# Performance work log

Measured on AMD Instinct MI355X. Metric: run time of the kernel, lower is better.

## Reference

```python
import jax, jax.numpy as jnp
import numpy as np

N = 32768   # total nodes
B = 128     # graphs
S = 256     # nodes per graph (equal-size graphs)
E = 524288  # edges
DIN = 128   # in_dim
DH = 256    # hidden_dim
H = 8       # heads
DFF = 1024  # ffn hidden
EPS = 1e-5


def _seg_sum(x, idx, num):
    return jax.ops.segment_sum(x, idx, num_segments=num)


def _bn(x, g, b):
    # BatchNorm1d with batch statistics (training-mode math, deterministic)
    mu = jnp.mean(x, axis=0)
    var = jnp.mean((x - mu) ** 2, axis=0)
    return (x - mu) * jax.lax.rsqrt(var + EPS) * g + b


def _ln(x, g, b):
    mu = jnp.mean(x, axis=-1, keepdims=True)
    var = jnp.mean((x - mu) ** 2, axis=-1, keepdims=True)
    return (x - mu) * jax.lax.rsqrt(var + EPS) * g + b


def _gcn_conv(x, W, bias, edge_index, n):
    # PyG GCNConv: h = x W; add self-loops; norm = d^-1/2[row] * d^-1/2[col]; scatter-add at col
    h = x @ W
    loop = jnp.arange(n)
    row = jnp.concatenate([edge_index[0], loop])
    col = jnp.concatenate([edge_index[1], loop])
    deg = _seg_sum(jnp.ones_like(col, dtype=h.dtype), col, n)  # >=1 due to self-loops
    dis = jax.lax.rsqrt(jnp.maximum(deg, 1.0))
    norm = dis[row] * dis[col]
    out = _seg_sum(h[row] * norm[:, None], col, n)
    return out + bias


def setup_inputs() -> dict:
    key = jax.random.key(0)
    ks = jax.random.split(key, 24)

    def w(i, shape, scale=0.05):
        return jax.random.normal(ks[i], shape, dtype=jnp.float32) * scale

    return {
        "x": jax.random.normal(ks[0], (N, DIN), dtype=jnp.float32),
        "edge_index": jax.random.randint(ks[1], (2, E), 0, N, dtype=jnp.int32),
        "batch": jnp.repeat(jnp.arange(B, dtype=jnp.int32), S),
        "inter_f": jax.random.normal(ks[2], (B, DH), dtype=jnp.float32),
        "bn1_g": jnp.ones((DIN,), jnp.float32), "bn1_b": jnp.zeros((DIN,), jnp.float32),
        "bn2_g": jnp.ones((DH,), jnp.float32), "bn2_b": jnp.zeros((DH,), jnp.float32),
        "w_conv1": w(3, (DIN, DH)), "b_conv1": jnp.zeros((DH,), jnp.float32),
        "w_conv2": w(4, (DH, DH)), "b_conv2": jnp.zeros((DH,), jnp.float32),
        "wq": w(5, (DH, DH)), "bq": jnp.zeros((DH,), jnp.float32),
        "wk": w(6, (DH, DH)), "bk": jnp.zeros((DH,), jnp.float32),
        "wv": w(7, (DH, DH)), "bv": jnp.zeros((DH,), jnp.float32),
        "wo": w(8, (DH, DH)), "bo": jnp.zeros((DH,), jnp.float32),
        "ln1_g": jnp.ones((DH,), jnp.float32), "ln1_b": jnp.zeros((DH,), jnp.float32),
        "ln2_g": jnp.ones((DH,), jnp.float32), "ln2_b": jnp.zeros((DH,), jnp.float32),
        "w_ff1": w(9, (DH, DFF)), "b_ff1": jnp.zeros((DFF,), jnp.float32),
        "w_ff2": w(10, (DFF, DH)), "b_ff2": jnp.zeros((DH,), jnp.float32),
    }


def reference(x, edge_index, batch, inter_f,
              bn1_g, bn1_b, bn2_g, bn2_b,
              w_conv1, b_conv1, w_conv2, b_conv2,
              wq, bq, wk, bk, wv, bv, wo, bo,
              ln1_g, ln1_b, ln2_g, ln2_b,
              w_ff1, b_ff1, w_ff2, b_ff2):
    n = x.shape[0]
    hd = DH // H
    # init_avg_h: scatter-mean of raw x per graph
    cnt = _seg_sum(jnp.ones((n,), x.dtype), batch, B)
    init_avg_h = _seg_sum(x, batch, B) / jnp.maximum(cnt, 1.0)[:, None]
    # layer 1 (dropout = identity in eval)
    h = _bn(x, bn1_g, bn1_b)
    h = jax.nn.relu(_gcn_conv(h, w_conv1, b_conv1, edge_index, n))
    # layer 2 with residual
    pre = h
    h2 = _bn(h, bn2_g, bn2_b)
    h = pre + jax.nn.relu(_gcn_conv(h2, w_conv2, b_conv2, edge_index, n))
    # transformer block: inject per-graph feature, self-attend within each graph
    inter_h = inter_f[batch]
    t = (h + inter_h).reshape(B, S, DH)
    q = (t @ wq + bq).reshape(B, S, H, hd)
    k = (t @ wk + bk).reshape(B, S, H, hd)
    v = (t @ wv + bv).reshape(B, S, H, hd)
    scores = jnp.einsum('bqhd,bkhd->bhqk', q, k) / jnp.sqrt(jnp.float32(hd))
    attn = jax.nn.softmax(scores, axis=-1)
    o = jnp.einsum('bhqk,bkhd->bqhd', attn, v).reshape(B, S, DH) @ wo + bo
    t2 = _ln(t + o, ln1_g, ln1_b)
    ffn = jax.nn.relu(t2 @ w_ff1 + b_ff1) @ w_ff2 + b_ff2
    t3 = _ln(t2 + ffn, ln2_g, ln2_b)
    hg = t3.reshape(n, DH)
    readout = _seg_sum(hg, batch, B)
    return readout, init_avg_h
```

## Files before the change

kernel.cpp:

```cpp
#include <hip/hip_runtime.h>
#include <math.h>

#define NN   32768
#define BG   128
#define SG   256
#define EE   524288
#define DIN_ 128
#define DH_  256
#define NH   8
#define HD_  32
#define DFF_ 1024
#define EPS_ 1e-5f

typedef __attribute__((ext_vector_type(8))) short bf16x8;
typedef __attribute__((ext_vector_type(4))) float f32x4;
typedef __attribute__((ext_vector_type(2))) unsigned int u32x2;
typedef __attribute__((ext_vector_type(4))) unsigned int u32x4;

__device__ __forceinline__ unsigned short f2bf(float f) {
    unsigned int u = __builtin_bit_cast(unsigned int, f);
    unsigned int r = u + 0x7FFFu + ((u >> 16) & 1u);
    return (unsigned short)(r >> 16);
}
__device__ __forceinline__ float bf2f(unsigned short u) {
    return __builtin_bit_cast(float, (unsigned int)u << 16);
}
__device__ __forceinline__ unsigned int pack2bf(float a, float b) {
    return (unsigned int)f2bf(a) | ((unsigned int)f2bf(b) << 16);
}
__device__ __forceinline__ void glds16(const unsigned short* g, unsigned short* l) {
    __builtin_amdgcn_global_load_lds(
        (const __attribute__((address_space(1))) void*)g,
        (__attribute__((address_space(3))) void*)l, 16, 0, 0);
}
#define WAIT_VM2() __builtin_amdgcn_s_waitcnt(0x0F72)
#define WAIT_VM1() __builtin_amdgcn_s_waitcnt(0x0F71)
#define WAIT_VM0() __builtin_amdgcn_s_waitcnt(0x0F70)

#define QSCALE (0.17677669529663689f * 1.4426950408889634f)

__global__ __launch_bounds__(128) void initavg_kernel(const float* __restrict__ X,
                                                      float* __restrict__ out2) {
    int b = blockIdx.x, j = threadIdx.x;
    float s = 0.f;
    for (int r = 0; r < SG; ++r) s += X[(size_t)(b * SG + r) * DIN_ + j];
    out2[b * DIN_ + j] = s * (1.f / (float)SG);
}

template <int C>
__global__ __launch_bounds__(C) void colstats_kernel(const float* __restrict__ X,
                                                     float* __restrict__ csum,
                                                     float* __restrict__ csumsq) {
    int j = threadIdx.x;
    size_t r0 = (size_t)blockIdx.x * 256;
    float s = 0.f, sq = 0.f;
    for (int r = 0; r < 256; ++r) {
        float v = X[(r0 + r) * C + j];
        s += v; sq += v * v;
    }
    atomicAdd(&csum[j], s);
    atomicAdd(&csumsq[j], sq);
}

template <int C>
__global__ __launch_bounds__(C) void colstats_b_kernel(const unsigned short* __restrict__ X,
                                                       float* __restrict__ csum,
                                                       float* __restrict__ csumsq) {
    int j = threadIdx.x;
    size_t r0 = (size_t)blockIdx.x * 256;
    float s = 0.f, sq = 0.f;
    for (int r = 0; r < 256; ++r) {
        float v = bf2f(X[(r0 + r) * C + j]);
        s += v; sq += v * v;
    }
    atomicAdd(&csum[j], s);
    atomicAdd(&csumsq[j], sq);
}

template <int C>
__global__ __launch_bounds__(C) void bnfin_kernel(const float* __restrict__ csum,
                                                  const float* __restrict__ csumsq,
                                                  const float* __restrict__ g,
                                                  const float* __restrict__ b,
                                                  float* __restrict__ scale,
                                                  float* __restrict__ shift) {
    int j = threadIdx.x;
    float mu  = csum[j] * (1.f / (float)NN);
    float var = csumsq[j] * (1.f / (float)NN) - mu * mu;
    float s = g[j] * rsqrtf(var + EPS_);
    scale[j] = s;
    shift[j] = b[j] - mu * s;
}

template <int C>
__global__ __launch_bounds__(256) void bnapply_kernel(const float* __restrict__ X,
                                                      const float* __restrict__ sc,
                                                      const float* __restrict__ sh,
                                                      unsigned short* __restrict__ Y) {
    int i = blockIdx.x * 256 + threadIdx.x;
    int j = i & (C - 1);
    Y[i] = f2bf(X[i] * sc[j] + sh[j]);
}

__global__ __launch_bounds__(256) void wtrans_kernel(const float* __restrict__ W,
                                                     unsigned short* __restrict__ Wt,
                                                     int K, int N, float scale) {
    int idx = blockIdx.x * 256 + threadIdx.x;
    if (idx < K * N) {
        int n = idx / K, k = idx - n * K;
        Wt[idx] = f2bf(W[(size_t)k * N + n] * scale);
    }
}

__global__ __launch_bounds__(256) void bcat_kernel(const float* __restrict__ bq,
                                                   const float* __restrict__ bk,
                                                   const float* __restrict__ bv,
                                                   float* __restrict__ o) {
    int j = threadIdx.x;
    if (blockIdx.x == 0) o[j] = bq[j] * QSCALE;
    else if (blockIdx.x == 1) o[DH_ + j] = bk[j];
    else o[2 * DH_ + j] = bv[j];
}

__global__ __launch_bounds__(256) void deg_kernel(const int* __restrict__ col,
                                                  int* __restrict__ deg) {
    int e = blockIdx.x * 256 + threadIdx.x;
    if (e < EE) atomicAdd(&deg[col[e]], 1);
}

__global__ __launch_bounds__(1024) void scan_kernel(const int* __restrict__ deg,
                                                    int* __restrict__ off,
                                                    float* __restrict__ dis) {
    __shared__ int sums[1024];
    int t = threadIdx.x;
    int base = t * 32;
    int loc[32];
    int run = 0;
#pragma unroll
    for (int i = 0; i < 32; ++i) { loc[i] = run; run += deg[base + i]; }
    sums[t] = run;
    __syncthreads();
    for (int d = 1; d < 1024; d <<= 1) {
        int tmp = (t >= d) ? sums[t - d] : 0;
        __syncthreads();
        sums[t] += tmp;
        __syncthreads();
    }
    int excl = sums[t] - run;
#pragma unroll
    for (int i = 0; i < 32; ++i) {
        off[base + i] = excl + loc[i];
        dis[base + i] = rsqrtf((float)(deg[base + i] + 1));
    }
    if (t == 1023) off[NN] = sums[1023];
}

__global__ __launch_bounds__(256) void scatter_kernel(const int* __restrict__ row,
                                                      const int* __restrict__ col,
                                                      const int* __restrict__ off,
                                                      int* __restrict__ cnt,
                                                      int* __restrict__ srow) {
    int e = blockIdx.x * 256 + threadIdx.x;
    if (e < EE) {
        int c = col[e];
        int p = off[c] + atomicAdd(&cnt[c], 1);
        srow[p] = row[e];
    }
}

template <int C, int FUSE_BN>
__global__ __launch_bounds__(256) void aggb_kernel(const unsigned short* __restrict__ X,
                                                   const int* __restrict__ off,
                                                   const int* __restrict__ srow,
                                                   const float* __restrict__ dis,
                                                   const float* __restrict__ scl,
                                                   const float* __restrict__ shf,
                                                   unsigned short* __restrict__ Y) {
    constexpr int EPL = C / 64;
    int lane = threadIdx.x & 63;
    int c = blockIdx.x * 4 + (threadIdx.x >> 6);
    float dc = dis[c];
    float acc[EPL];
    float wsum = dc;
    {
        unsigned short t[EPL];
        const unsigned short* xc = X + (size_t)c * C + lane * EPL;
        if constexpr (EPL == 4) *(uint2*)t = *(const uint2*)xc;
        else *(unsigned int*)t = *(const unsigned int*)xc;
#pragma unroll
        for (int e2 = 0; e2 < EPL; ++e2) acc[e2] = dc * bf2f(t[e2]);
    }
    int s = off[c], en = off[c + 1];
    int i = s;
    for (; i + 4 <= en; i += 4) {
        int r0 = srow[i], r1 = srow[i + 1], r2 = srow[i + 2], r3 = srow[i + 3];
        float d0 = dis[r0], d1 = dis[r1], d2 = dis[r2], d3 = dis[r3];
        unsigned short t0[EPL], t1[EPL], t2[EPL], t3[EPL];
        const unsigned short* p0 = X + (size_t)r0 * C + lane * EPL;
        const unsigned short* p1 = X + (size_t)r1 * C + lane * EPL;
        const unsigned short* p2 = X + (size_t)r2 * C + lane * EPL;
        const unsigned short* p3 = X + (size_t)r3 * C + lane * EPL;
        if constexpr (EPL == 4) {
            *(uint2*)t0 = *(const uint2*)p0;
            *(uint2*)t1 = *(const uint2*)p1;
            *(uint2*)t2 = *(const uint2*)p2;
            *(uint2*)t3 = *(const uint2*)p3;
        } else {
            *(unsigned int*)t0 = *(const unsigned int*)p0;
            *(unsigned int*)t1 = *(const unsigned int*)p1;
            *(unsigned int*)t2 = *(const unsigned int*)p2;
            *(unsigned int*)t3 = *(const unsigned int*)p3;
        }
        wsum += d0 + d1 + d2 + d3;
#pragma unroll
        for (int e2 = 0; e2 < EPL; ++e2) {
            acc[e2] += d0 * bf2f(t0[e2]) + d1 * bf2f(t1[e2]) +
                       d2 * bf2f(t2[e2]) + d3 * bf2f(t3[e2]);
        }
    }
    for (; i < en; ++i) {
        int r = srow[i];
        float dr = dis[r];
        unsigned short t[EPL];
        const unsigned short* xr = X + (size_t)r * C + lane * EPL;
        if constexpr (EPL == 4) *(uint2*)t = *(const uint2*)xr;
        else *(unsigned int*)t = *(const unsigned int*)xr;
        wsum += dr;
#pragma unroll
        for (int e2 = 0; e2 < EPL; ++e2) acc[e2] += dr * bf2f(t[e2]);
    }
    unsigned short t[EPL];
#pragma unroll
    for (int e2 = 0; e2 < EPL; ++e2) {
        float v;
        if constexpr (FUSE_BN) {
            int j = lane * EPL + e2;
            v = dc * (scl[j] * acc[e2] + shf[j] * wsum);
        } else {
            v = dc * acc[e2];
        }
        t[e2] = f2bf(v);
    }
    unsigned short* yc = Y + (size_t)c * C + lane * EPL;
    if constexpr (EPL == 4) *(uint2*)yc = *(const uint2*)t;
    else *(unsigned int*)yc = *(const unsigned int*)t;
}

template <int MT>
__global__ __launch_bounds__(512, 8) void gemm_bf16_kernel(
    const unsigned short* __restrict__ A,
    const unsigned short* __restrict__ Bt,
    unsigned short* __restrict__ Cb,
    int M, int K, int N,
    const float* __restrict__ bias,
    const unsigned short* __restrict__ resb,
    const float* __restrict__ inter,
    int do_relu, int relu_first) {
    constexpr int LDP = 32;
    constexpr int CP = 136;
    constexpr int MI = MT / 64;
    constexpr int ASZ = MT * 32;
    constexpr int SMEMSZ = (MT == 128) ? 128 * CP : 2 * ASZ + 2 * 4096;
    __shared__ unsigned short Smem[SMEMSZ];
    unsigned short* As0 = Smem;
    unsigned short* As1 = Smem + ASZ;
    unsigned short* Bs0 = Smem + 2 * ASZ;
    unsigned short* Bs1 = Smem + 2 * ASZ + 4096;
    unsigned short* Cs  = Smem;
    int gx = gridDim.x, gyP = gridDim.y >> 3;
    int d = blockIdx.y * gx + blockIdx.x;
    int xcd = d & 7, j2 = d >> 3;
    int bm = (xcd * gyP + j2 / gx) * MT;
    int bn = (j2 % gx) * 128;
    int tid = threadIdx.x;
    int wave = tid >> 6, lane = tid & 63;
    int wm = (wave >> 1) * (MT / 4);
    int wn = (wave & 1) * 64;
    int lrc = lane & 15;
    int koct = lane >> 4;
    int rsw = (lrc >> 1) & 3;
    int rofs = (koct ^ rsw) * 8;

    int cg = (lane & 3) ^ ((lane >> 3) & 3);
    int skk = cg * 8;
    const unsigned short* g0 = nullptr;
    unsigned short* l0a = nullptr;
    unsigned short* l0b = nullptr;
    int nloads;
    size_t gstride16;
    if constexpr (MT == 128) {
        int sr = wave * 16 + (lane >> 2);
        g0 = A + (size_t)(bm + sr) * K + skk;
        nloads = 2;
        (void)l0a; (void)l0b; (void)gstride16;
    } else {
        if (wave < 4) {
            int sr = wave * 32 + (lane >> 2);
            g0 = Bt + (size_t)(bn + sr) * K + skk;
            l0a = Bs0 + wave * 1024 + lane * 8;
            l0b = Bs1 + wave * 1024 + lane * 8;
            nloads = 2;
            gstride16 = (size_t)16 * K;
        } else {
            int sr = (wave - 4) * 16 + (lane >> 2);
            g0 = A + (size_t)(bm + sr) * K + skk;
            l0a = As0 + (wave - 4) * 512 + lane * 8;
            l0b = As1 + (wave - 4) * 512 + lane * 8;
            nloads = 1;
            gstride16 = 0;
        }
    }
    const unsigned short* gA0 = nullptr;
    const unsigned short* gB0 = nullptr;
    int lofs = 0;
    if constexpr (MT == 128) {
        int sr = wave * 16 + (lane >> 2);
        gA0 = A + (size_t)(bm + sr) * K + skk;
        gB0 = Bt + (size_t)(bn + sr) * K + skk;
        lofs = wave * 512 + lane * 8;
    }

    f32x4 acc[MI][4];
#pragma unroll
    for (int i = 0; i < MI; ++i)
#pragma unroll
        for (int j = 0; j < 4; ++j) acc[i][j] = (f32x4){0.f, 0.f, 0.f, 0.f};

    if constexpr (MT == 128) {
        glds16(gA0, As0 + lofs);
        glds16(gB0, Bs0 + lofs);
    } else {
        glds16(g0, l0a);
        if (nloads == 2) glds16(g0 + gstride16, l0a + 512);
    }

    int buf = 0;
    for (int k0 = 0; k0 < K; k0 += 32) {
        int nk = k0 + 32;
        if (nk < K) {
            if constexpr (MT == 128) {
                glds16(gA0 + nk, (buf ? As0 : As1) + lofs);
                glds16(gB0 + nk, (buf ? Bs0 : Bs1) + lofs);
                WAIT_VM2();
            } else {
                unsigned short* ln = buf ? l0a : l0b;
                glds16(g0 + nk, ln);
                if (nloads == 2) {
                    glds16(g0 + nk + gstride16, ln + 512);
                    WAIT_VM2();
                } else {
                    WAIT_VM1();
                }
            }
        } else {
            WAIT_VM0();
        }
        __builtin_amdgcn_s_barrier();
        const unsigned short* Ab = buf ? As1 : As0;
        const unsigned short* Bb = buf ? Bs1 : Bs0;
        bf16x8 af[MI], bfr[4];
#pragma unroll
        for (int i = 0; i < MI; ++i)
            af[i] = *(const bf16x8*)(Ab + (wm + i * 16 + lrc) * LDP + rofs);
#pragma unroll
        for (int j = 0; j < 4; ++j)
            bfr[j] = *(const bf16x8*)(Bb + (wn + j * 16 + lrc) * LDP + rofs);
#pragma unroll
        for (int i = 0; i < MI; ++i)
#pragma unroll
            for (int j = 0; j < 4; ++j)
                acc[i][j] = __builtin_amdgcn_mfma_f32_16x16x32_bf16(af[i], bfr[j],
                                                                    acc[i][j], 0, 0, 0);
        __builtin_amdgcn_s_barrier();
        buf ^= 1;
    }
#pragma unroll
    for (int i = 0; i < MI; ++i) {
#pragma unroll
        for (int r = 0; r < 4; ++r) {
            int lrow = wm + i * 16 + koct * 4 + r;
            int grow = bm + lrow;
#pragma unroll
            for (int j = 0; j < 4; ++j) {
                int lcol = wn + j * 16 + lrc;
                int gcol = bn + lcol;
                float v = acc[i][j][r];
                if (bias) v += bias[gcol];
                if (relu_first) v = fmaxf(v, 0.f);
                if (resb) v += bf2f(resb[(size_t)grow * N + gcol]);
                if (inter) v += inter[(grow >> 8) * N + gcol];
                if (do_relu && !relu_first) v = fmaxf(v, 0.f);
                Cs[lrow * CP + lcol] = f2bf(v);
            }
        }
    }
    __syncthreads();
#pragma unroll
    for (int it = 0; it < MT / 32; ++it) {
        int row = it * 32 + (tid >> 4);
        int cc = (tid & 15) * 8;
        *(uint4*)(&Cb[(size_t)(bm + row) * N + bn + cc]) =
            *(const uint4*)(&Cs[row * CP + cc]);
    }
}

__global__ __launch_bounds__(256, 4) void attn_mfma_kernel(
    const unsigned short* __restrict__ QKV,
    unsigned short* __restrict__ Ob) {
    int b = blockIdx.x >> 3, h = blockIdx.x & 7;
    __shared__ unsigned short Ks[256 * 32];
    __shared__ unsigned short Vt[32 * 264];
    __shared__ float Lc[4 * 64];
    const unsigned short* kg = QKV + (size_t)b * 256 * 768 + 256 + h * 32;
    const unsigned short* vg = QKV + (size_t)b * 256 * 768 + 512 + h * 32;
    int tid = threadIdx.x;
#pragma unroll
    for (int it = 0; it < 4; ++it) {
        int c = it * 256 + tid;
        int row = c >> 2, ch = c & 3;
        int slot = ch ^ ((row >> 1) & 3);
        *(uint4*)(Ks + row * 32 + slot * 8) =
            *(const uint4*)(kg + (size_t)row * 768 + ch * 8);
    }
#pragma unroll
    for (int it = 0; it < 4; ++it) {
        int c = it * 256 + tid;
        int key = c >> 2, d0 = (c & 3) * 8;
        unsigned short tmp[8];
        *(uint4*)tmp = *(const uint4*)(vg + (size_t)key * 768 + d0);
#pragma unroll
        for (int j = 0; j < 8; ++j) Vt[(d0 + j) * 264 + key] = tmp[j];
    }
    __syncthreads();

    int wave = tid >> 6, lane = tid & 63;
    int lr = lane & 15, koct = lane >> 4;
    int s4 = (lr >> 1) & 3;
    int qrow0 = b * 256 + wave * 64;
    bf16x8 qf[4];
#pragma unroll
    for (int j = 0; j < 4; ++j)
        qf[j] = *(const bf16x8*)(QKV + (size_t)(qrow0 + j * 16 + lr) * 768 + h * 32 + koct * 8);

    f32x4 Oa[4][2];
    float lp[4];
#pragma unroll
    for (int i = 0; i < 4; ++i) {
        Oa[i][0] = (f32x4){0.f, 0.f, 0.f, 0.f};
        Oa[i][1] = (f32x4){0.f, 0.f, 0.f, 0.f};
        lp[i] = 0.f;
    }
    float* Lw = Lc + wave * 64;

    for (int kc = 0; kc < 256; kc += 32) {
        bf16x8 kf0 = *(const bf16x8*)(Ks + (kc + lr) * 32 + (koct ^ s4) * 8);
        bf16x8 kf1 = *(const bf16x8*)(Ks + (kc + 16 + lr) * 32 + (koct ^ s4) * 8);
        bf16x8 pfr[4];
#pragma unroll
        for (int j = 0; j < 4; ++j) {
            f32x4 St0 = __builtin_amdgcn_mfma_f32_16x16x32_bf16(kf0, qf[j],
                            (f32x4){0.f, 0.f, 0.f, 0.f}, 0, 0, 0);
            f32x4 St1 = __builtin_amdgcn_mfma_f32_16x16x32_bf16(kf1, qf[j],
                            (f32x4){0.f, 0.f, 0.f, 0.f}, 0, 0, 0);
            float p0[4], p1[4], ps = 0.f;
#pragma unroll
            for (int r = 0; r < 4; ++r) {
                p0[r] = exp2f(St0[r]); p1[r] = exp2f(St1[r]);
                ps += p0[r] + p1[r];
            }
            lp[j] += ps;
            unsigned int w0a, w0b, w1a, w1b;
            asm("v_cvt_pk_bf16_f32 %0, %1, %2" : "=v"(w0a) : "v"(p0[0]), "v"(p0[1]));
            asm("v_cvt_pk_bf16_f32 %0, %1, %2" : "=v"(w0b) : "v"(p0[2]), "v"(p0[3]));
            asm("v_cvt_pk_bf16_f32 %0, %1, %2" : "=v"(w1a) : "v"(p1[0]), "v"(p1[1]));
            asm("v_cvt_pk_bf16_f32 %0, %1, %2" : "=v"(w1b) : "v"(p1[2]), "v"(p1[3]));
            u32x2 sa = __builtin_amdgcn_permlane32_swap(w0a, w1a, false, false);
            u32x2 da = __builtin_amdgcn_permlane16_swap(sa[0], sa[1], false, false);
            u32x2 sb = __builtin_amdgcn_permlane32_swap(w0b, w1b, false, false);
            u32x2 db = __builtin_amdgcn_permlane16_swap(sb[0], sb[1], false, false);
            u32x4 pw = {da[0], db[0], da[1], db[1]};
            pfr[j] = __builtin_bit_cast(bf16x8, pw);
        }
        bf16x8 vf0 = *(const bf16x8*)(Vt + lr * 264 + kc + koct * 8);
        bf16x8 vf1 = *(const bf16x8*)(Vt + (16 + lr) * 264 + kc + koct * 8);
#pragma unroll
        for (int i = 0; i < 4; ++i) {
            Oa[i][0] = __builtin_amdgcn_mfma_f32_16x16x32_bf16(pfr[i], vf0, Oa[i][0], 0, 0, 0);
            Oa[i][1] = __builtin_amdgcn_mfma_f32_16x16x32_bf16(pfr[i], vf1, Oa[i][1], 0, 0, 0);
        }
    }
#pragma unroll
    for (int j = 0; j < 4; ++j) {
        lp[j] += __shfl_xor(lp[j], 16);
        lp[j] += __shfl_xor(lp[j], 32);
    }
    if (koct == 0) {
#pragma unroll
        for (int j = 0; j < 4; ++j) Lw[j * 16 + lr] = lp[j];
    }
    __builtin_amdgcn_s_waitcnt(0);
#pragma unroll
    for (int i = 0; i < 4; ++i) {
        f32x4 l4 = *(const f32x4*)(Lw + i * 16 + koct * 4);
#pragma unroll
        for (int r = 0; r < 4; ++r) {
            float inv = 1.f / l4[r];
            int row = qrow0 + i * 16 + koct * 4 + r;
#pragma unroll
            for (int jn = 0; jn < 2; ++jn) {
                int col = h * 32 + jn * 16 + lr;
                Ob[(size_t)row * 256 + col] = f2bf(Oa[i][jn][r] * inv);
            }
        }
    }
}

__global__ __launch_bounds__(256) void lnb_kernel(const unsigned short* __restrict__ Z,
                                                  unsigned short* __restrict__ Out,
                                                  const float* __restrict__ g,
                                                  const float* __restrict__ bt) {
    int row = blockIdx.x * 4 + (threadIdx.x >> 6);
    int lane = threadIdx.x & 63;
    const unsigned short* z = Z + (size_t)row * DH_;
    float v[4];
    float sum = 0.f;
#pragma unroll
    for (int i = 0; i < 4; ++i) { v[i] = bf2f(z[lane + i * 64]); sum += v[i]; }
#pragma unroll
    for (int off = 32; off; off >>= 1) sum += __shfl_xor(sum, off);
    float mu = sum * (1.f / (float)DH_);
    float vs = 0.f;
#pragma unroll
    for (int i = 0; i < 4; ++i) { float d = v[i] - mu; vs += d * d; }
#pragma unroll
    for (int off = 32; off; off >>= 1) vs += __shfl_xor(vs, off);
    float rs = rsqrtf(vs * (1.f / (float)DH_) + EPS_);
#pragma unroll
    for (int i = 0; i < 4; ++i) {
        int col = lane + i * 64;
        Out[(size_t)row * DH_ + col] = f2bf((v[i] - mu) * rs * g[col] + bt[col]);
    }
}

__global__ __launch_bounds__(256) void readout_kernel(const unsigned short* __restrict__ T3,
                                                      float* __restrict__ out) {
    int b = blockIdx.x, j = threadIdx.x;
    float s = 0.f;
    for (int r = 0; r < SG; ++r) s += bf2f(T3[(size_t)(b * SG + r) * DH_ + j]);
    out[b * DH_ + j] = s;
}

extern "C" void kernel_launch(void* const* d_in, const int* in_sizes, int n_in,
                              void* d_out, int out_size, void* d_ws, size_t ws_size,
                              hipStream_t stream) {
    const float* x       = (const float*)d_in[0];
    const int*   ei      = (const int*)d_in[1];
    const float* inter_f = (const float*)d_in[3];
    const float* bn1_g = (const float*)d_in[4],  *bn1_b = (const float*)d_in[5];
    const float* bn2_g = (const float*)d_in[6],  *bn2_b = (const float*)d_in[7];
    const float* w_conv1 = (const float*)d_in[8],  *b_conv1 = (const float*)d_in[9];
    const float* w_conv2 = (const float*)d_in[10], *b_conv2 = (const float*)d_in[11];
    const float* wq = (const float*)d_in[12], *bq = (const float*)d_in[13];
    const float* wk = (const float*)d_in[14], *bk = (const float*)d_in[15];
    const float* wv = (const float*)d_in[16], *bv = (const float*)d_in[17];
    const float* wo = (const float*)d_in[18], *bo = (const float*)d_in[19];
    const float* ln1_g = (const float*)d_in[20], *ln1_b = (const float*)d_in[21];
    const float* ln2_g = (const float*)d_in[22], *ln2_b = (const float*)d_in[23];
    const float* w_ff1 = (const float*)d_in[24], *b_ff1 = (const float*)d_in[25];
    const float* w_ff2 = (const float*)d_in[26], *b_ff2 = (const float*)d_in[27];
    float* out = (float*)d_out;

    char* base = (char*)d_ws;
    size_t o = 0;
    auto alloc = [&](size_t bytes) -> void* {
        void* p = base + o;
        o = (o + bytes + 255) & ~(size_t)255;
        return p;
    };
    int*   deg    = (int*)alloc(NN * 4);
    int*   off    = (int*)alloc((NN + 1) * 4);
    int*   cnt    = (int*)alloc(NN * 4);
    int*   srow   = (int*)alloc(EE * 4);
    float* dis    = (float*)alloc(NN * 4);
    float* csum   = (float*)alloc(256 * 4);
    float* csumsq = (float*)alloc(256 * 4);
    float* scl    = (float*)alloc(256 * 4);
    float* shf    = (float*)alloc(256 * 4);
    float* bqkv   = (float*)alloc(768 * 4);
    const size_t SLOT = (size_t)NN * DH_;
    unsigned short* Arena = (unsigned short*)alloc((size_t)NN * DFF_ * 2);
    unsigned short* TB = (unsigned short*)alloc(SLOT * 2);
    unsigned short* B0 = (unsigned short*)alloc(SLOT * 2);
    unsigned short* wc1t  = (unsigned short*)alloc((size_t)DIN_ * DH_ * 2);
    unsigned short* wc2t  = (unsigned short*)alloc((size_t)DH_ * DH_ * 2);
    unsigned short* wqkvt = (unsigned short*)alloc((size_t)DH_ * DH_ * 3 * 2);
    unsigned short* wot   = (unsigned short*)alloc((size_t)DH_ * DH_ * 2);
    unsigned short* wf1t  = (unsigned short*)alloc((size_t)DH_ * DFF_ * 2);
    unsigned short* wf2t  = (unsigned short*)alloc((size_t)DFF_ * DH_ * 2);
    unsigned short* Xa   = Arena;
    unsigned short* X2a  = Arena + (size_t)NN * DIN_;
    unsigned short* QKVb = Arena;
    unsigned short* zb   = Arena + SLOT * 3;
    unsigned short* Fb   = Arena;
    unsigned short* tb   = TB;
    unsigned short* z2b  = TB;

    hipMemsetAsync(deg, 0, NN * 4, stream);
    hipMemsetAsync(cnt, 0, NN * 4, stream);
    hipMemsetAsync(csum, 0, 2048, stream);

    wtrans_kernel<<<(DIN_ * DH_ + 255) / 256, 256, 0, stream>>>(w_conv1, wc1t, DIN_, DH_, 1.f);
    wtrans_kernel<<<(DH_ * DH_ + 255) / 256, 256, 0, stream>>>(w_conv2, wc2t, DH_, DH_, 1.f);
    wtrans_kernel<<<(DH_ * DH_ + 255) / 256, 256, 0, stream>>>(wq, wqkvt, DH_, DH_, QSCALE);
    wtrans_kernel<<<(DH_ * DH_ + 255) / 256, 256, 0, stream>>>(wk, wqkvt + DH_ * DH_, DH_, DH_, 1.f);
    wtrans_kernel<<<(DH_ * DH_ + 255) / 256, 256, 0, stream>>>(wv, wqkvt + 2 * DH_ * DH_, DH_, DH_, 1.f);
    wtrans_kernel<<<(DH_ * DH_ + 255) / 256, 256, 0, stream>>>(wo, wot, DH_, DH_, 1.f);
    wtrans_kernel<<<(DH_ * DFF_ + 255) / 256, 256, 0, stream>>>(w_ff1, wf1t, DH_, DFF_, 1.f);
    wtrans_kernel<<<(DFF_ * DH_ + 255) / 256, 256, 0, stream>>>(w_ff2, wf2t, DFF_, DH_, 1.f);
    bcat_kernel<<<3, 256, 0, stream>>>(bq, bk, bv, bqkv);

    initavg_kernel<<<BG, 128, 0, stream>>>(x, out + BG * DH_);

    colstats_kernel<DIN_><<<NN / 256, DIN_, 0, stream>>>(x, csum, csumsq);
    bnfin_kernel<DIN_><<<1, DIN_, 0, stream>>>(csum, csumsq, bn1_g, bn1_b, scl, shf);
    bnapply_kernel<DIN_><<<NN * DIN_ / 256, 256, 0, stream>>>(x, scl, shf, B0);

    deg_kernel<<<EE / 256, 256, 0, stream>>>(ei + EE, deg);
    scan_kernel<<<1, 1024, 0, stream>>>(deg, off, dis);
    scatter_kernel<<<EE / 256, 256, 0, stream>>>(ei, ei + EE, off, cnt, srow);

    aggb_kernel<DIN_, 0><<<NN / 4, 256, 0, stream>>>(B0, off, srow, dis,
                                                     nullptr, nullptr, Xa);
    gemm_bf16_kernel<64><<<dim3(DH_ / 128, NN / 64), 512, 0, stream>>>(
        Xa, wc1t, B0, NN, DIN_, DH_, b_conv1, nullptr, nullptr, 1, 0);

    hipMemsetAsync(csum, 0, 2048, stream);
    colstats_b_kernel<DH_><<<NN / 256, DH_, 0, stream>>>(B0, csum, csumsq);
    bnfin_kernel<DH_><<<1, DH_, 0, stream>>>(csum, csumsq, bn2_g, bn2_b, scl, shf);

    aggb_kernel<DH_, 1><<<NN / 4, 256, 0, stream>>>(B0, off, srow, dis,
                                                    scl, shf, X2a);
    gemm_bf16_kernel<64><<<dim3(DH_ / 128, NN / 64), 512, 0, stream>>>(
        X2a, wc2t, tb, NN, DH_, DH_, b_conv2, B0, inter_f, 1, 1);

    gemm_bf16_kernel<128><<<dim3(768 / 128, NN / 128), 512, 0, stream>>>(
        tb, wqkvt, QKVb, NN, DH_, 768, bqkv, nullptr, nullptr, 0, 0);

    attn_mfma_kernel<<<BG * NH, 256, 0, stream>>>(QKVb, B0);

    gemm_bf16_kernel<64><<<dim3(DH_ / 128, NN / 64), 512, 0, stream>>>(
        B0, wot, zb, NN, DH_, DH_, bo, tb, nullptr, 0, 0);
    lnb_kernel<<<NN / 4, 256, 0, stream>>>(zb, B0, ln1_g, ln1_b);

    gemm_bf16_kernel<128><<<dim3(DFF_ / 128, NN / 128), 512, 0, stream>>>(
        B0, wf1t, Fb, NN, DH_, DFF_, b_ff1, nullptr, nullptr, 1, 0);
    gemm_bf16_kernel<64><<<dim3(DH_ / 128, NN / 64), 512, 0, stream>>>(
        Fb, wf2t, z2b, NN, DFF_, DH_, b_ff2, B0, nullptr, 0, 0);

    lnb_kernel<<<NN / 4, 256, 0, stream>>>(z2b, B0, ln2_g, ln2_b);
    readout_kernel<<<BG, 256, 0, stream>>>(B0, out);
}
```

Measured before the change: 541.7 us.

## Triple-buffer MT=64 GEMM loads and vectorize layernorm row access

The MT=64 GEMM path moves from double to triple buffering in LDS, issuing global-to-LDS loads two K-steps ahead with adjusted waitcnt thresholds. This hides more global-load latency behind the MFMA work. It raises LDS use per block, which may lower occupancy. Separately, the layernorm kernel now loads and stores four contiguous bf16 values per lane and reads gamma and beta as float4, replacing strided scalar accesses.

```diff
diff --git a/kernel.cpp b/kernel.cpp
--- a/kernel.cpp
+++ b/kernel.cpp
@@ -33,6 +33,7 @@
         (const __attribute__((address_space(1))) void*)g,
         (__attribute__((address_space(3))) void*)l, 16, 0, 0);
 }
+#define WAIT_VM4() __builtin_amdgcn_s_waitcnt(0x0F74)
 #define WAIT_VM2() __builtin_amdgcn_s_waitcnt(0x0F72)
 #define WAIT_VM1() __builtin_amdgcn_s_waitcnt(0x0F71)
 #define WAIT_VM0() __builtin_amdgcn_s_waitcnt(0x0F70)
@@ -259,14 +260,10 @@
     constexpr int LDP = 32;
     constexpr int CP = 136;
     constexpr int MI = MT / 64;
-    constexpr int ASZ = MT * 32;
-    constexpr int SMEMSZ = (MT == 128) ? 128 * CP : 2 * ASZ + 2 * 4096;
+    constexpr int STG = 6144;
+    constexpr int SMEMSZ = (MT == 128) ? 128 * CP : 3 * STG;
     __shared__ unsigned short Smem[SMEMSZ];
-    unsigned short* As0 = Smem;
-    unsigned short* As1 = Smem + ASZ;
-    unsigned short* Bs0 = Smem + 2 * ASZ;
-    unsigned short* Bs1 = Smem + 2 * ASZ + 4096;
-    unsigned short* Cs  = Smem;
+    unsigned short* Cs = Smem;
     int gx = gridDim.x, gyP = gridDim.y >> 3;
     int d = blockIdx.y * gx + blockIdx.x;
     int xcd = d & 7, j2 = d >> 3;
@@ -283,37 +280,31 @@
 
     int cg = (lane & 3) ^ ((lane >> 3) & 3);
     int skk = cg * 8;
+
     const unsigned short* g0 = nullptr;
-    unsigned short* l0a = nullptr;
-    unsigned short* l0b = nullptr;
-    int nloads;
-    size_t gstride16;
-    if constexpr (MT == 128) {
-        int sr = wave * 16 + (lane >> 2);
-        g0 = A + (size_t)(bm + sr) * K + skk;
-        nloads = 2;
-        (void)l0a; (void)l0b; (void)gstride16;
-    } else {
+    int lofs64 = 0;
+    int nloads = 2;
+    size_t gstride16 = 0;
+    if constexpr (MT == 64) {
         if (wave < 4) {
             int sr = wave * 32 + (lane >> 2);
             g0 = Bt + (size_t)(bn + sr) * K + skk;
-            l0a = Bs0 + wave * 1024 + lane * 8;
-            l0b = Bs1 + wave * 1024 + lane * 8;
+            lofs64 = 2048 + wave * 1024 + lane * 8;
             nloads = 2;
             gstride16 = (size_t)16 * K;
         } else {
             int sr = (wave - 4) * 16 + (lane >> 2);
             g0 = A + (size_t)(bm + sr) * K + skk;
-            l0a = As0 + (wave - 4) * 512 + lane * 8;
-            l0b = As1 + (wave - 4) * 512 + lane * 8;
+            lofs64 = (wave - 4) * 512 + lane * 8;
             nloads = 1;
-            gstride16 = 0;
         }
     }
     const unsigned short* gA0 = nullptr;
     const unsigned short* gB0 = nullptr;
     int lofs = 0;
+    unsigned short *As0 = nullptr, *As1 = nullptr, *Bs0 = nullptr, *Bs1 = nullptr;
     if constexpr (MT == 128) {
+        As0 = Smem; As1 = Smem + 4096; Bs0 = Smem + 8192; Bs1 = Smem + 12288;
         int sr = wave * 16 + (lane >> 2);
         gA0 = A + (size_t)(bm + sr) * K + skk;
         gB0 = Bt + (size_t)(bn + sr) * K + skk;
@@ -330,34 +321,50 @@
         glds16(gA0, As0 + lofs);
         glds16(gB0, Bs0 + lofs);
     } else {
-        glds16(g0, l0a);
-        if (nloads == 2) glds16(g0 + gstride16, l0a + 512);
-    }
-
-    int buf = 0;
+        glds16(g0, Smem + lofs64);
+        if (nloads == 2) glds16(g0 + gstride16, Smem + lofs64 + 512);
+        glds16(g0 + 32, Smem + STG + lofs64);
+        if (nloads == 2) glds16(g0 + 32 + gstride16, Smem + STG + lofs64 + 512);
+    }
+
+    int buf = 0, rb = 0;
     for (int k0 = 0; k0 < K; k0 += 32) {
-        int nk = k0 + 32;
-        if (nk < K) {
-            if constexpr (MT == 128) {
+        if constexpr (MT == 128) {
+            int nk = k0 + 32;
+            if (nk < K) {
                 glds16(gA0 + nk, (buf ? As0 : As1) + lofs);
                 glds16(gB0 + nk, (buf ? Bs0 : Bs1) + lofs);
                 WAIT_VM2();
             } else {
-                unsigned short* ln = buf ? l0a : l0b;
-                glds16(g0 + nk, ln);
-                if (nloads == 2) {
-                    glds16(g0 + nk + gstride16, ln + 512);
-                    WAIT_VM2();
-                } else {
-                    WAIT_VM1();
-                }
+                WAIT_VM0();
             }
         } else {
-            WAIT_VM0();
+            if (k0 + 64 < K) {
+                int wb = rb + 2; if (wb >= 3) wb -= 3;
+                unsigned short* ld = Smem + wb * STG + lofs64;
+                glds16(g0 + k0 + 64, ld);
+                if (nloads == 2) {
+                    glds16(g0 + k0 + 64 + gstride16, ld + 512);
+                    WAIT_VM4();
+                } else {
+                    WAIT_VM2();
+                }
+            } else if (k0 + 32 < K) {
+                if (nloads == 2) WAIT_VM2(); else WAIT_VM1();
+            } else {
+                WAIT_VM0();
+            }
         }
         __builtin_amdgcn_s_barrier();
-        const unsigned short* Ab = buf ? As1 : As0;
-        const unsigned short* Bb = buf ? Bs1 : Bs0;
+        const unsigned short* Ab;
+        const unsigned short* Bb;
+        if constexpr (MT == 128) {
+            Ab = buf ? As1 : As0;
+            Bb = buf ? Bs1 : Bs0;
+        } else {
+            Ab = Smem + rb * STG;
+            Bb = Ab + 2048;
+        }
         bf16x8 af[MI], bfr[4];
 #pragma unroll
         for (int i = 0; i < MI; ++i)
@@ -372,7 +379,8 @@
                 acc[i][j] = __builtin_amdgcn_mfma_f32_16x16x32_bf16(af[i], bfr[j],
                                                                     acc[i][j], 0, 0, 0);
         __builtin_amdgcn_s_barrier();
-        buf ^= 1;
+        if constexpr (MT == 128) buf ^= 1;
+        else rb = (rb + 1 == 3) ? 0 : rb + 1;
     }
 #pragma unroll
     for (int i = 0; i < MI; ++i) {
@@ -521,25 +529,29 @@
                                                   const float* __restrict__ bt) {
     int row = blockIdx.x * 4 + (threadIdx.x >> 6);
     int lane = threadIdx.x & 63;
-    const unsigned short* z = Z + (size_t)row * DH_;
+    unsigned short tv[4];
+    *(uint2*)tv = *(const uint2*)(Z + (size_t)row * DH_ + lane * 4);
     float v[4];
     float sum = 0.f;
 #pragma unroll
-    for (int i = 0; i < 4; ++i) { v[i] = bf2f(z[lane + i * 64]); sum += v[i]; }
+    for (int i = 0; i < 4; ++i) { v[i] = bf2f(tv[i]); sum += v[i]; }
 #pragma unroll
     for (int off = 32; off; off >>= 1) sum += __shfl_xor(sum, off);
     float mu = sum * (1.f / (float)DH_);
     float vs = 0.f;
 #pragma unroll
-    for (int i = 0; i < 4; ++i) { float d = v[i] - mu; vs += d * d; }
+    for (int i = 0; i < 4; ++i) { float dd = v[i] - mu; vs += dd * dd; }
 #pragma unroll
     for (int off = 32; off; off >>= 1) vs += __shfl_xor(vs, off);
     float rs = rsqrtf(vs * (1.f / (float)DH_) + EPS_);
-#pragma unroll
-    for (int i = 0; i < 4; ++i) {
-        int col = lane + i * 64;
-        Out[(size_t)row * DH_ + col] = f2bf((v[i] - mu) * rs * g[col] + bt[col]);
-    }
+    float4 gv = *(const float4*)(g + lane * 4);
+    float4 bv = *(const float4*)(bt + lane * 4);
+    unsigned short ov[4];
+    ov[0] = f2bf((v[0] - mu) * rs * gv.x + bv.x);
+    ov[1] = f2bf((v[1] - mu) * rs * gv.y + bv.y);
+    ov[2] = f2bf((v[2] - mu) * rs * gv.z + bv.z);
+    ov[3] = f2bf((v[3] - mu) * rs * gv.w + bv.w);
+    *(uint2*)(Out + (size_t)row * DH_ + lane * 4) = *(uint2*)ov;
 }
 
 __global__ __launch_bounds__(256) void readout_kernel(const unsigned short* __restrict__ T3,
```

Measured after the change: 533.9 us. No clear change (-1.4%).
